# Performance work log

Hardware: AMD Instinct MI355X
Metric: run time of the kernel (lower is better)

## Reference

```python
import jax, jax.numpy as jnp
import numpy as np

EMB = 1024
HEADS = 16
HEAD_SIZE = EMB // HEADS  # 64
B, T = 2, 2048


def setup_inputs() -> dict:
    key = jax.random.key(0)
    k1, k2, k3 = jax.random.split(key, 3)
    x = jax.random.normal(k1, (B, T, EMB), dtype=jnp.float32)
    # scale weights like typical init to keep logits sane
    w_qkv = jax.random.normal(k2, (EMB, 3 * EMB), dtype=jnp.float32) * (EMB ** -0.5)
    w_proj = jax.random.normal(k3, (EMB, EMB), dtype=jnp.float32) * (EMB ** -0.5)
    b_proj = jnp.zeros((EMB,), dtype=jnp.float32)
    return {"x": x, "w_qkv": w_qkv, "w_proj": w_proj, "b_proj": b_proj}


def reference(x, w_qkv, w_proj, b_proj):
    Bb, Tt, C = x.shape
    qkv = x @ w_qkv  # [B,T,3C]
    q, k, v = jnp.split(qkv, 3, axis=-1)
    # [B,H,T,hs]
    q = q.reshape(Bb, Tt, HEADS, HEAD_SIZE).transpose(0, 2, 1, 3)
    k = k.reshape(Bb, Tt, HEADS, HEAD_SIZE).transpose(0, 2, 1, 3)
    v = v.reshape(Bb, Tt, HEADS, HEAD_SIZE).transpose(0, 2, 1, 3)
    scale = HEAD_SIZE ** -0.5
    wei = jnp.einsum('bhqd,bhkd->bhqk', q, k) * scale  # [B,H,T,T]
    causal = jnp.tril(jnp.ones((Tt, Tt), dtype=bool))
    wei = jnp.where(causal, wei, -jnp.inf)
    wei = jax.nn.softmax(wei, axis=-1)
    out = jnp.einsum('bhqk,bhkd->bhqd', wei, v)  # [B,H,T,hs]
    out = out.transpose(0, 2, 1, 3).reshape(Bb, Tt, C)
    out = out @ w_proj + b_proj
    return out
```

## Files before the change

### kernel.cpp

```cpp
#include <hip/hip_runtime.h>
#include <hip/hip_bf16.h>

typedef __attribute__((ext_vector_type(8))) short short8;
typedef __attribute__((ext_vector_type(4))) float floatx4;

#define MFMA16(a, b, c) __builtin_amdgcn_mfma_f32_16x16x32_bf16((a), (b), (c), 0, 0, 0)
#define GLOBAL_AS __attribute__((address_space(1)))
#define LDS_AS __attribute__((address_space(3)))

__device__ __forceinline__ unsigned short f2bf(float x) {
  union { float f; unsigned u; } v; v.f = x;
  unsigned r = v.u + 0x7FFFu + ((v.u >> 16) & 1u);
  return (unsigned short)(r >> 16);
}

__device__ __forceinline__ short8 ld8(const unsigned short* p) {
  return *reinterpret_cast<const short8*>(p);
}

__device__ __forceinline__ void async_cp16(const unsigned short* g, unsigned short* l) {
  __builtin_amdgcn_global_load_lds((const GLOBAL_AS void*)g, (LDS_AS void*)l, 16, 0, 0);
}

__global__ __launch_bounds__(256) void k_prep(
    const float* __restrict__ x, unsigned short* __restrict__ xb,
    const float* __restrict__ w_qkv, unsigned short* __restrict__ wqkvT,
    const float* __restrict__ w_proj, unsigned short* __restrict__ wprojT) {
  __shared__ float tile[64][65];
  int bid = blockIdx.x, tid = threadIdx.x;
  if (bid < 4096) {
    int i = bid * 256 + tid;
    float4 f = reinterpret_cast<const float4*>(x)[i];
    union { unsigned short u[4]; unsigned long long v; } o;
    o.u[0] = f2bf(f.x); o.u[1] = f2bf(f.y); o.u[2] = f2bf(f.z); o.u[3] = f2bf(f.w);
    reinterpret_cast<unsigned long long*>(xb)[i] = o.v;
    return;
  }
  const float* in; unsigned short* out; int R, C, bx, by;
  if (bid < 4864) {
    int rel = bid - 4096;
    in = w_qkv; out = wqkvT; R = 1024; C = 3072; bx = rel % 48; by = rel / 48;
  } else {
    int rel = bid - 4864;
    in = w_proj; out = wprojT; R = 1024; C = 1024; bx = rel % 16; by = rel / 16;
  }
  int tx = tid & 63, ty = tid >> 6;
  int c0 = bx * 64, r0 = by * 64;
  for (int i = ty; i < 64; i += 4)
    tile[i][tx] = in[(size_t)(r0 + i) * C + c0 + tx];
  __syncthreads();
  for (int i = ty; i < 64; i += 4)
    out[(size_t)(c0 + i) * R + r0 + tx] = f2bf(tile[tx][i]);
}

__global__ __launch_bounds__(256) void k_gemm_qkv(
    const unsigned short* __restrict__ A, const unsigned short* __restrict__ Bt,
    unsigned short* __restrict__ qk, unsigned short* __restrict__ vT, int K) {
  __shared__ unsigned short As[128][64];
  __shared__ unsigned short Bs[128][64];
  int tid = threadIdx.x;
  int w = tid >> 6, lane = tid & 63, quad = lane >> 4, l16 = lane & 15;
  int wy = w >> 1, wx = w & 1;
  int rowB = blockIdx.y * 128, colB = blockIdx.x * 128;
  int srcRow = lane >> 3;
  int srcCol = (((lane & 7) ^ (srcRow & 7)) << 3);

  floatx4 acc[4][4];
  floatx4 zero4 = {0.f, 0.f, 0.f, 0.f};
#pragma unroll
  for (int mi = 0; mi < 4; ++mi)
#pragma unroll
    for (int ni = 0; ni < 4; ++ni) acc[mi][ni] = zero4;

  for (int kt = 0; kt < K; kt += 64) {
    __syncthreads();
#pragma unroll
    for (int i = 0; i < 4; ++i) {
      int r0 = w * 32 + i * 8;
      async_cp16(&A[(size_t)(rowB + r0 + srcRow) * K + kt + srcCol], &As[r0][0]);
      async_cp16(&Bt[(size_t)(colB + r0 + srcRow) * K + kt + srcCol], &Bs[r0][0]);
    }
    __syncthreads();
#pragma unroll
    for (int kh = 0; kh < 2; ++kh) {
      short8 af[4], bf_[4];
#pragma unroll
      for (int mi = 0; mi < 4; ++mi)
        af[mi] = ld8(&As[wy * 64 + mi * 16 + l16][((kh * 4 + quad) ^ (l16 & 7)) << 3]);
#pragma unroll
      for (int ni = 0; ni < 4; ++ni)
        bf_[ni] = ld8(&Bs[wx * 64 + ni * 16 + l16][((kh * 4 + quad) ^ (l16 & 7)) << 3]);
#pragma unroll
      for (int mi = 0; mi < 4; ++mi)
#pragma unroll
        for (int ni = 0; ni < 4; ++ni)
          acc[mi][ni] = MFMA16(af[mi], bf_[ni], acc[mi][ni]);
    }
  }

  if (colB < 2048) {
#pragma unroll
    for (int mi = 0; mi < 4; ++mi) {
      int row = rowB + wy * 64 + mi * 16 + quad * 4;
#pragma unroll
      for (int ni = 0; ni < 4; ++ni) {
        int col = colB + wx * 64 + ni * 16 + l16;
#pragma unroll
        for (int r = 0; r < 4; ++r)
          qk[(size_t)(row + r) * 2048 + col] = f2bf(acc[mi][ni][r]);
      }
    }
  } else {
#pragma unroll
    for (int mi = 0; mi < 4; ++mi) {
      int row = rowB + wy * 64 + mi * 16 + quad * 4;
      int b = row >> 11, t = row & 2047;
#pragma unroll
      for (int ni = 0; ni < 4; ++ni) {
        int hd = colB - 2048 + wx * 64 + ni * 16 + l16;
        union { unsigned short u[4]; unsigned long long v; } o;
#pragma unroll
        for (int r = 0; r < 4; ++r) o.u[r] = f2bf(acc[mi][ni][r]);
        *reinterpret_cast<unsigned long long*>(
            &vT[((size_t)(b * 16) * 64 + hd) * 2048 + t]) = o.v;
      }
    }
  }
}

__global__ __launch_bounds__(256) void k_gemm_proj(
    const unsigned short* __restrict__ A, const unsigned short* __restrict__ Bt,
    float* __restrict__ Cout, const float* __restrict__ bias, int M, int N, int K) {
  __shared__ unsigned short As[128][64];
  __shared__ unsigned short Bs[64][64];
  int tid = threadIdx.x;
  int w = tid >> 6, lane = tid & 63, quad = lane >> 4, l16 = lane & 15;
  int rowB = blockIdx.y * 128, colB = blockIdx.x * 64;
  int srcRow = lane >> 3;
  int srcCol = (((lane & 7) ^ (srcRow & 7)) << 3);

  floatx4 acc[2][4];
  floatx4 zero4 = {0.f, 0.f, 0.f, 0.f};
#pragma unroll
  for (int mi = 0; mi < 2; ++mi)
#pragma unroll
    for (int ni = 0; ni < 4; ++ni) acc[mi][ni] = zero4;

  for (int kt = 0; kt < K; kt += 64) {
    __syncthreads();
#pragma unroll
    for (int i = 0; i < 4; ++i) {
      int r0 = w * 32 + i * 8;
      async_cp16(&A[(size_t)(rowB + r0 + srcRow) * K + kt + srcCol], &As[r0][0]);
    }
#pragma unroll
    for (int i = 0; i < 2; ++i) {
      int r0 = w * 16 + i * 8;
      async_cp16(&Bt[(size_t)(colB + r0 + srcRow) * K + kt + srcCol], &Bs[r0][0]);
    }
    __syncthreads();
#pragma unroll
    for (int kh = 0; kh < 2; ++kh) {
      short8 af[2], bf_[4];
#pragma unroll
      for (int mi = 0; mi < 2; ++mi)
        af[mi] = ld8(&As[w * 32 + mi * 16 + l16][((kh * 4 + quad) ^ (l16 & 7)) << 3]);
#pragma unroll
      for (int ni = 0; ni < 4; ++ni)
        bf_[ni] = ld8(&Bs[ni * 16 + l16][((kh * 4 + quad) ^ (l16 & 7)) << 3]);
#pragma unroll
      for (int mi = 0; mi < 2; ++mi)
#pragma unroll
        for (int ni = 0; ni < 4; ++ni)
          acc[mi][ni] = MFMA16(af[mi], bf_[ni], acc[mi][ni]);
    }
  }

#pragma unroll
  for (int mi = 0; mi < 2; ++mi) {
    int row = rowB + w * 32 + mi * 16 + quad * 4;
#pragma unroll
    for (int ni = 0; ni < 4; ++ni) {
      int col = colB + ni * 16 + l16;
      float bv = bias[col];
#pragma unroll
      for (int r = 0; r < 4; ++r)
        Cout[(size_t)(row + r) * N + col] = acc[mi][ni][r] + bv;
    }
  }
}

__global__ __launch_bounds__(256) void k_attn(
    const unsigned short* __restrict__ qk, const unsigned short* __restrict__ vT,
    unsigned short* __restrict__ attn_out) {
  const int T = 2048, LD = 2048;
  __shared__ unsigned short Kt[128][72];
  __shared__ unsigned short Vt[64][136];
  __shared__ unsigned short Pt[4][2][16][76];

  int idx = blockIdx.x;
  int ip = (idx >> 3) & 15;
  int bh = (idx & 7) | ((idx >> 7) << 3);
  int b = bh >> 4, h = bh & 15;
  int tid = threadIdx.x, w = tid >> 6, lane = tid & 63;
  int quad = lane >> 4, l16 = lane & 15;

  const unsigned short* Qp = qk + (size_t)b * T * LD + h * 64;
  const unsigned short* Kp = Qp + 1024;
  const unsigned short* Vp = vT + (size_t)bh * 64 * T;

  const int q0s[2] = {ip * 64, (31 - ip) * 64};
  const int last64[2] = {ip, 31 - ip};
  int nt = (33 - ip) >> 1;

  short8 aq[2][2];
#pragma unroll
  for (int m = 0; m < 2; ++m) {
    const unsigned short* qrow = Qp + (size_t)(q0s[m] + w * 16 + l16) * LD + quad * 8;
    aq[m][0] = ld8(qrow);
    aq[m][1] = ld8(qrow + 32);
  }

  short8 ones8;
  {
    unsigned short o = 0x3F80;
#pragma unroll
    for (int j = 0; j < 8; ++j) ones8[j] = (short)o;
  }

  const float cscale = 0.125f * 1.44269504f;
  floatx4 o_acc[2][4], l_acc[2];
  floatx4 zero4 = {0.f, 0.f, 0.f, 0.f};
#pragma unroll
  for (int m = 0; m < 2; ++m) {
    l_acc[m] = zero4;
#pragma unroll
    for (int nd = 0; nd < 4; ++nd) o_acc[m][nd] = zero4;
  }

  int skR = tid >> 3, skC = (tid & 7) << 3;
  int svR = tid >> 4, svC = (tid & 15) << 3;

  short8 kreg[4], vreg[4];
#pragma unroll
  for (int j = 0; j < 4; ++j) {
    kreg[j] = ld8(&Kp[(size_t)(skR + j * 32) * LD + skC]);
    vreg[j] = ld8(&Vp[(size_t)(svR + j * 16) * T + svC]);
  }

  for (int kt = 0; kt < nt; ++kt) {
    __syncthreads();
#pragma unroll
    for (int j = 0; j < 4; ++j) {
      *reinterpret_cast<short8*>(&Kt[skR + j * 32][skC]) = kreg[j];
      *reinterpret_cast<short8*>(&Vt[svR + j * 16][svC]) = vreg[j];
    }
    __syncthreads();

    if (kt + 1 < nt) {
      int key0n = (kt + 1) * 128;
#pragma unroll
      for (int j = 0; j < 4; ++j) {
        kreg[j] = ld8(&Kp[(size_t)(key0n + skR + j * 32) * LD + skC]);
        vreg[j] = ld8(&Vp[(size_t)(svR + j * 16) * T + key0n + svC]);
      }
    }

#pragma unroll
    for (int hh = 0; hh < 2; ++hh) {
      int half = kt * 2 + hh;
      if (half > last64[1]) continue;
      bool act0 = (half <= last64[0]);
      int key0 = half * 64;
      int ko = hh * 64;

      floatx4 st[2][4];
#pragma unroll
      for (int kt4 = 0; kt4 < 4; ++kt4) {
        short8 ak0 = ld8(&Kt[ko + kt4 * 16 + l16][quad * 8]);
        short8 ak1 = ld8(&Kt[ko + kt4 * 16 + l16][32 + quad * 8]);
        st[1][kt4] = MFMA16(ak0, aq[1][0], zero4);
        st[1][kt4] = MFMA16(ak1, aq[1][1], st[1][kt4]);
        if (act0) {
          st[0][kt4] = MFMA16(ak0, aq[0][0], zero4);
          st[0][kt4] = MFMA16(ak1, aq[0][1], st[0][kt4]);
        }
      }

#pragma unroll
      for (int m = 0; m < 2; ++m) {
        if (m == 0 && !act0) continue;
        if (half == last64[m]) {
          int qlane = q0s[m] + w * 16 + l16;
#pragma unroll
          for (int kt4 = 0; kt4 < 4; ++kt4)
#pragma unroll
            for (int r = 0; r < 4; ++r)
              if (key0 + kt4 * 16 + quad * 4 + r > qlane) st[m][kt4][r] = -1e30f;
        }
#pragma unroll
        for (int kt4 = 0; kt4 < 4; ++kt4) {
          unsigned u[4];
#pragma unroll
          for (int r = 0; r < 4; ++r) {
            float p = __builtin_amdgcn_exp2f(fmaf(st[m][kt4][r], cscale, -16.f));
            u[r] = __float_as_uint(p) + 0x8000u;
          }
          unsigned lo = __builtin_amdgcn_perm(u[1], u[0], 0x07060302u);
          unsigned hi = __builtin_amdgcn_perm(u[3], u[2], 0x07060302u);
          unsigned long long pv = ((unsigned long long)hi << 32) | lo;
          *reinterpret_cast<unsigned long long*>(
              &Pt[w][m][l16][kt4 * 16 + quad * 4]) = pv;
        }
      }

      short8 pa[2][2];
      pa[1][0] = ld8(&Pt[w][1][l16][quad * 8]);
      pa[1][1] = ld8(&Pt[w][1][l16][32 + quad * 8]);
      if (act0) {
        pa[0][0] = ld8(&Pt[w][0][l16][quad * 8]);
        pa[0][1] = ld8(&Pt[w][0][l16][32 + quad * 8]);
      }
#pragma unroll
      for (int nd = 0; nd < 4; ++nd) {
        short8 bv0 = ld8(&Vt[nd * 16 + l16][ko + quad * 8]);
        short8 bv1 = ld8(&Vt[nd * 16 + l16][ko + 32 + quad * 8]);
        o_acc[1][nd] = MFMA16(pa[1][0], bv0, o_acc[1][nd]);
        o_acc[1][nd] = MFMA16(pa[1][1], bv1, o_acc[1][nd]);
        if (act0) {
          o_acc[0][nd] = MFMA16(pa[0][0], bv0, o_acc[0][nd]);
          o_acc[0][nd] = MFMA16(pa[0][1], bv1, o_acc[0][nd]);
        }
      }
      l_acc[1] = MFMA16(pa[1][0], ones8, l_acc[1]);
      l_acc[1] = MFMA16(pa[1][1], ones8, l_acc[1]);
      if (act0) {
        l_acc[0] = MFMA16(pa[0][0], ones8, l_acc[0]);
        l_acc[0] = MFMA16(pa[0][1], ones8, l_acc[0]);
      }
    }
  }

#pragma unroll
  for (int m = 0; m < 2; ++m)
#pragma unroll
    for (int nd = 0; nd < 4; ++nd)
#pragma unroll
      for (int r = 0; r < 4; ++r) {
        int q = q0s[m] + w * 16 + quad * 4 + r;
        int d = nd * 16 + l16;
        attn_out[(size_t)(b * T + q) * 1024 + h * 64 + d] =
            f2bf(o_acc[m][nd][r] / l_acc[m][r]);
      }
}

extern "C" void kernel_launch(void* const* d_in, const int* in_sizes, int n_in,
                              void* d_out, int out_size, void* d_ws, size_t ws_size,
                              hipStream_t stream) {
  const float* x = (const float*)d_in[0];
  const float* w_qkv = (const float*)d_in[1];
  const float* w_proj = (const float*)d_in[2];
  const float* b_proj = (const float*)d_in[3];
  float* out = (float*)d_out;

  char* ws = (char*)d_ws;
  unsigned short* xb     = (unsigned short*)(ws);
  unsigned short* wqkvT  = (unsigned short*)(ws + (size_t)(8  << 20));
  unsigned short* wprojT = (unsigned short*)(ws + (size_t)(14 << 20));
  unsigned short* qkb    = (unsigned short*)(ws + (size_t)(16 << 20));
  unsigned short* attnb  = (unsigned short*)(ws + (size_t)(32 << 20));
  unsigned short* vTb    = (unsigned short*)(ws + (size_t)(40 << 20));

  k_prep<<<5120, 256, 0, stream>>>(x, xb, w_qkv, wqkvT, w_proj, wprojT);
  k_gemm_qkv<<<dim3(3072 / 128, 4096 / 128), 256, 0, stream>>>(
      xb, wqkvT, qkb, vTb, 1024);
  k_attn<<<512, 256, 0, stream>>>(qkb, vTb, attnb);
  k_gemm_proj<<<dim3(1024 / 64, 4096 / 128), 256, 0, stream>>>(
      attnb, wprojT, out, b_proj, 4096, 1024, 1024);
}
```

Before: 184.9 us.

## Split attention KV range across two blocks with split-K reduction via atomic counter

Each paired query tile's key range is split into two halves handled by separate blocks, doubling the grid to 1024 blocks. Each block writes unnormalized fp32 partial O and row sums to workspace. The second block to finish, detected by an atomic counter reset in the prep kernel, merges both partials and writes bf16 output. The KV tile shrinks to 64 keys to cut LDS use, and launch bounds request 4 blocks per SM. This aims at better occupancy and load balance at the cost of extra global traffic for the partials and a fence-plus-atomic reduction.

```diff
diff --git a/kernel.cpp b/kernel.cpp
--- a/kernel.cpp
+++ b/kernel.cpp
@@ -25,9 +25,14 @@
 __global__ __launch_bounds__(256) void k_prep(
     const float* __restrict__ x, unsigned short* __restrict__ xb,
     const float* __restrict__ w_qkv, unsigned short* __restrict__ wqkvT,
-    const float* __restrict__ w_proj, unsigned short* __restrict__ wprojT) {
+    const float* __restrict__ w_proj, unsigned short* __restrict__ wprojT,
+    int* __restrict__ counters) {
   __shared__ float tile[64][65];
   int bid = blockIdx.x, tid = threadIdx.x;
+  if (bid == 0) {
+    counters[tid] = 0;
+    counters[tid + 256] = 0;
+  }
   if (bid < 4096) {
     int i = bid * 256 + tid;
     float4 f = reinterpret_cast<const float4*>(x)[i];
@@ -190,18 +195,24 @@
   }
 }
 
-__global__ __launch_bounds__(256) void k_attn(
+__global__ __launch_bounds__(256, 4) void k_attn(
     const unsigned short* __restrict__ qk, const unsigned short* __restrict__ vT,
-    unsigned short* __restrict__ attn_out) {
+    unsigned short* __restrict__ attn_out,
+    float* __restrict__ o_part, float* __restrict__ l_part,
+    int* __restrict__ counters) {
   const int T = 2048, LD = 2048;
-  __shared__ unsigned short Kt[128][72];
-  __shared__ unsigned short Vt[64][136];
+  __shared__ unsigned short Kt[64][72];
+  __shared__ unsigned short Vt[64][72];
   __shared__ unsigned short Pt[4][2][16][76];
+  __shared__ int done;
 
   int idx = blockIdx.x;
-  int ip = (idx >> 3) & 15;
-  int bh = (idx & 7) | ((idx >> 7) << 3);
+  int hf = (idx >> 3) & 1;
+  int ip = (idx >> 4) & 15;
+  int bh = (idx & 7) | ((idx >> 8) << 3);
   int b = bh >> 4, h = bh & 15;
+  int pid = bh * 16 + ip;
+  int slot = pid * 2 + hf;
   int tid = threadIdx.x, w = tid >> 6, lane = tid & 63;
   int quad = lane >> 4, l16 = lane & 15;
 
@@ -211,7 +222,10 @@
 
   const int q0s[2] = {ip * 64, (31 - ip) * 64};
   const int last64[2] = {ip, 31 - ip};
-  int nt = (33 - ip) >> 1;
+  int NH = 32 - ip;
+  int hsplit = (ip >= 8) ? 9 : 16 - ip;
+  int h0 = hf ? hsplit : 0;
+  int h1 = hf ? NH : hsplit;
 
   short8 aq[2][2];
 #pragma unroll
@@ -239,119 +253,148 @@
   }
 
   int skR = tid >> 3, skC = (tid & 7) << 3;
-  int svR = tid >> 4, svC = (tid & 15) << 3;
-
-  short8 kreg[4], vreg[4];
-#pragma unroll
-  for (int j = 0; j < 4; ++j) {
-    kreg[j] = ld8(&Kp[(size_t)(skR + j * 32) * LD + skC]);
-    vreg[j] = ld8(&Vp[(size_t)(svR + j * 16) * T + svC]);
-  }
-
-  for (int kt = 0; kt < nt; ++kt) {
-    __syncthreads();
-#pragma unroll
-    for (int j = 0; j < 4; ++j) {
+
+  short8 kreg[2], vreg[2];
+#pragma unroll
+  for (int j = 0; j < 2; ++j) {
+    kreg[j] = ld8(&Kp[(size_t)(h0 * 64 + skR + j * 32) * LD + skC]);
+    vreg[j] = ld8(&Vp[(size_t)(skR + j * 32) * T + h0 * 64 + skC]);
+  }
+
+  for (int half = h0; half < h1; ++half) {
+    __syncthreads();
+#pragma unroll
+    for (int j = 0; j < 2; ++j) {
       *reinterpret_cast<short8*>(&Kt[skR + j * 32][skC]) = kreg[j];
-      *reinterpret_cast<short8*>(&Vt[svR + j * 16][svC]) = vreg[j];
-    }
-    __syncthreads();
-
-    if (kt + 1 < nt) {
-      int key0n = (kt + 1) * 128;
-#pragma unroll
-      for (int j = 0; j < 4; ++j) {
+      *reinterpret_cast<short8*>(&Vt[skR + j * 32][skC]) = vreg[j];
+    }
+    __syncthreads();
+
+    if (half + 1 < h1) {
+      int key0n = (half + 1) * 64;
+#pragma unroll
+      for (int j = 0; j < 2; ++j) {
         kreg[j] = ld8(&Kp[(size_t)(key0n + skR + j * 32) * LD + skC]);
-        vreg[j] = ld8(&Vp[(size_t)(svR + j * 16) * T + key0n + svC]);
-      }
-    }
-
-#pragma unroll
-    for (int hh = 0; hh < 2; ++hh) {
-      int half = kt * 2 + hh;
-      if (half > last64[1]) continue;
-      bool act0 = (half <= last64[0]);
-      int key0 = half * 64;
-      int ko = hh * 64;
-
-      floatx4 st[2][4];
+        vreg[j] = ld8(&Vp[(size_t)(skR + j * 32) * T + key0n + skC]);
+      }
+    }
+
+    bool act0 = (half <= last64[0]);
+    int key0 = half * 64;
+
+    floatx4 st[2][4];
+#pragma unroll
+    for (int kt4 = 0; kt4 < 4; ++kt4) {
+      short8 ak0 = ld8(&Kt[kt4 * 16 + l16][quad * 8]);
+      short8 ak1 = ld8(&Kt[kt4 * 16 + l16][32 + quad * 8]);
+      st[1][kt4] = MFMA16(ak0, aq[1][0], zero4);
+      st[1][kt4] = MFMA16(ak1, aq[1][1], st[1][kt4]);
+      if (act0) {
+        st[0][kt4] = MFMA16(ak0, aq[0][0], zero4);
+        st[0][kt4] = MFMA16(ak1, aq[0][1], st[0][kt4]);
+      }
+    }
+
+#pragma unroll
+    for (int m = 0; m < 2; ++m) {
+      if (m == 0 && !act0) continue;
+      if (half == last64[m]) {
+        int qlane = q0s[m] + w * 16 + l16;
+#pragma unroll
+        for (int kt4 = 0; kt4 < 4; ++kt4)
+#pragma unroll
+          for (int r = 0; r < 4; ++r)
+            if (key0 + kt4 * 16 + quad * 4 + r > qlane) st[m][kt4][r] = -1e30f;
+      }
 #pragma unroll
       for (int kt4 = 0; kt4 < 4; ++kt4) {
-        short8 ak0 = ld8(&Kt[ko + kt4 * 16 + l16][quad * 8]);
-        short8 ak1 = ld8(&Kt[ko + kt4 * 16 + l16][32 + quad * 8]);
-        st[1][kt4] = MFMA16(ak0, aq[1][0], zero4);
-        st[1][kt4] = MFMA16(ak1, aq[1][1], st[1][kt4]);
-        if (act0) {
-          st[0][kt4] = MFMA16(ak0, aq[0][0], zero4);
-          st[0][kt4] = MFMA16(ak1, aq[0][1], st[0][kt4]);
+        unsigned u[4];
+#pragma unroll
+        for (int r = 0; r < 4; ++r) {
+          float p = __builtin_amdgcn_exp2f(fmaf(st[m][kt4][r], cscale, -16.f));
+          u[r] = __float_as_uint(p) + 0x8000u;
         }
-      }
-
-#pragma unroll
-      for (int m = 0; m < 2; ++m) {
-        if (m == 0 && !act0) continue;
-        if (half == last64[m]) {
-          int qlane = q0s[m] + w * 16 + l16;
-#pragma unroll
-          for (int kt4 = 0; kt4 < 4; ++kt4)
-#pragma unroll
-            for (int r = 0; r < 4; ++r)
-              if (key0 + kt4 * 16 + quad * 4 + r > qlane) st[m][kt4][r] = -1e30f;
-        }
-#pragma unroll
-        for (int kt4 = 0; kt4 < 4; ++kt4) {
-          unsigned u[4];
-#pragma unroll
-          for (int r = 0; r < 4; ++r) {
-            float p = __builtin_amdgcn_exp2f(fmaf(st[m][kt4][r], cscale, -16.f));
-            u[r] = __float_as_uint(p) + 0x8000u;
-          }
-          unsigned lo = __builtin_amdgcn_perm(u[1], u[0], 0x07060302u);
-          unsigned hi = __builtin_amdgcn_perm(u[3], u[2], 0x07060302u);
-          unsigned long long pv = ((unsigned long long)hi << 32) | lo;
-          *reinterpret_cast<unsigned long long*>(
-              &Pt[w][m][l16][kt4 * 16 + quad * 4]) = pv;
-        }
-      }
-
-      short8 pa[2][2];
-      pa[1][0] = ld8(&Pt[w][1][l16][quad * 8]);
-      pa[1][1] = ld8(&Pt[w][1][l16][32 + quad * 8]);
+        unsigned lo = __builtin_amdgcn_perm(u[1], u[0], 0x07060302u);
+        unsigned hi = __builtin_amdgcn_perm(u[3], u[2], 0x07060302u);
+        unsigned long long pv = ((unsigned long long)hi << 32) | lo;
+        *reinterpret_cast<unsigned long long*>(
+            &Pt[w][m][l16][kt4 * 16 + quad * 4]) = pv;
+      }
+    }
+
+    short8 pa[2][2];
+    pa[1][0] = ld8(&Pt[w][1][l16][quad * 8]);
+    pa[1][1] = ld8(&Pt[w][1][l16][32 + quad * 8]);
+    if (act0) {
+      pa[0][0] = ld8(&Pt[w][0][l16][quad * 8]);
+      pa[0][1] = ld8(&Pt[w][0][l16][32 + quad * 8]);
+    }
+#pragma unroll
+    for (int nd = 0; nd < 4; ++nd) {
+      short8 bv0 = ld8(&Vt[nd * 16 + l16][quad * 8]);
+      short8 bv1 = ld8(&Vt[nd * 16 + l16][32 + quad * 8]);
+      o_acc[1][nd] = MFMA16(pa[1][0], bv0, o_acc[1][nd]);
+      o_acc[1][nd] = MFMA16(pa[1][1], bv1, o_acc[1][nd]);
       if (act0) {
-        pa[0][0] = ld8(&Pt[w][0][l16][quad * 8]);
-        pa[0][1] = ld8(&Pt[w][0][l16][32 + quad * 8]);
-      }
-#pragma unroll
-      for (int nd = 0; nd < 4; ++nd) {
-        short8 bv0 = ld8(&Vt[nd * 16 + l16][ko + quad * 8]);
-        short8 bv1 = ld8(&Vt[nd * 16 + l16][ko + 32 + quad * 8]);
-        o_acc[1][nd] = MFMA16(pa[1][0], bv0, o_acc[1][nd]);
-        o_acc[1][nd] = MFMA16(pa[1][1], bv1, o_acc[1][nd]);
-        if (act0) {
-          o_acc[0][nd] = MFMA16(pa[0][0], bv0, o_acc[0][nd]);
-          o_acc[0][nd] = MFMA16(pa[0][1], bv1, o_acc[0][nd]);
-        }
-      }
-      l_acc[1] = MFMA16(pa[1][0], ones8, l_acc[1]);
-      l_acc[1] = MFMA16(pa[1][1], ones8, l_acc[1]);
-      if (act0) {
-        l_acc[0] = MFMA16(pa[0][0], ones8, l_acc[0]);
-        l_acc[0] = MFMA16(pa[0][1], ones8, l_acc[0]);
-      }
-    }
-  }
-
+        o_acc[0][nd] = MFMA16(pa[0][0], bv0, o_acc[0][nd]);
+        o_acc[0][nd] = MFMA16(pa[0][1], bv1, o_acc[0][nd]);
+      }
+    }
+    l_acc[1] = MFMA16(pa[1][0], ones8, l_acc[1]);
+    l_acc[1] = MFMA16(pa[1][1], ones8, l_acc[1]);
+    if (act0) {
+      l_acc[0] = MFMA16(pa[0][0], ones8, l_acc[0]);
+      l_acc[0] = MFMA16(pa[0][1], ones8, l_acc[0]);
+    }
+  }
+
+  float* OP = o_part + (size_t)slot * (2 * 64 * 64);
+  float* LP = l_part + (size_t)slot * (2 * 64);
 #pragma unroll
   for (int m = 0; m < 2; ++m)
 #pragma unroll
     for (int nd = 0; nd < 4; ++nd)
 #pragma unroll
-      for (int r = 0; r < 4; ++r) {
-        int q = q0s[m] + w * 16 + quad * 4 + r;
-        int d = nd * 16 + l16;
-        attn_out[(size_t)(b * T + q) * 1024 + h * 64 + d] =
-            f2bf(o_acc[m][nd][r] / l_acc[m][r]);
-      }
+      for (int r = 0; r < 4; ++r)
+        OP[(m * 64 + w * 16 + quad * 4 + r) * 64 + nd * 16 + l16] = o_acc[m][nd][r];
+  if (l16 == 0)
+#pragma unroll
+    for (int m = 0; m < 2; ++m)
+#pragma unroll
+      for (int r = 0; r < 4; ++r)
+        LP[m * 64 + w * 16 + quad * 4 + r] = l_acc[m][r];
+
+  __threadfence();
+  __syncthreads();
+  if (tid == 0) done = atomicAdd(&counters[pid], 1);
+  __syncthreads();
+  if (done != 1) return;
+
+  __threadfence();
+  const float* PA = o_part + (size_t)(pid * 2) * (2 * 64 * 64);
+  const float* PB = PA + 2 * 64 * 64;
+  const float* LA = l_part + (size_t)(pid * 2) * (2 * 64);
+  const float* LB = LA + 2 * 64;
+#pragma unroll
+  for (int m = 0; m < 2; ++m) {
+    int qg0 = q0s[m];
+#pragma unroll
+    for (int pass = 0; pass < 4; ++pass) {
+      int q = pass * 16 + (tid >> 4);
+      int d0 = (tid & 15) * 4;
+      int off = (m * 64 + q) * 64 + d0;
+      float4 a = *reinterpret_cast<const float4*>(&PA[off]);
+      float4 c = *reinterpret_cast<const float4*>(&PB[off]);
+      float rl = 1.0f / (LA[m * 64 + q] + LB[m * 64 + q]);
+      union { unsigned short u[4]; unsigned long long v; } ob;
+      ob.u[0] = f2bf((a.x + c.x) * rl);
+      ob.u[1] = f2bf((a.y + c.y) * rl);
+      ob.u[2] = f2bf((a.z + c.z) * rl);
+      ob.u[3] = f2bf((a.w + c.w) * rl);
+      *reinterpret_cast<unsigned long long*>(
+          &attn_out[(size_t)(b * T + qg0 + q) * 1024 + h * 64 + d0]) = ob.v;
+    }
+  }
 }
 
 extern "C" void kernel_launch(void* const* d_in, const int* in_sizes, int n_in,
@@ -370,11 +413,14 @@
   unsigned short* qkb    = (unsigned short*)(ws + (size_t)(16 << 20));
   unsigned short* attnb  = (unsigned short*)(ws + (size_t)(32 << 20));
   unsigned short* vTb    = (unsigned short*)(ws + (size_t)(40 << 20));
-
-  k_prep<<<5120, 256, 0, stream>>>(x, xb, w_qkv, wqkvT, w_proj, wprojT);
+  float*          o_part = (float*)(ws + (size_t)(48 << 20));
+  float*          l_part = (float*)(ws + (size_t)(80 << 20));
+  int*            counters = (int*)(ws + (size_t)(80 << 20) + (512 << 10));
+
+  k_prep<<<5120, 256, 0, stream>>>(x, xb, w_qkv, wqkvT, w_proj, wprojT, counters);
   k_gemm_qkv<<<dim3(3072 / 128, 4096 / 128), 256, 0, stream>>>(
       xb, wqkvT, qkb, vTb, 1024);
-  k_attn<<<512, 256, 0, stream>>>(qkb, vTb, attnb);
+  k_attn<<<1024, 256, 0, stream>>>(qkb, vTb, attnb, o_part, l_part, counters);
   k_gemm_proj<<<dim3(1024 / 64, 4096 / 128), 256, 0, stream>>>(
       attnb, wprojT, out, b_proj, 4096, 1024, 1024);
 }
```

Result: slower. 414.1 us (+124.0%).

## Split paired causal attention blocks into one 64-row query tile per block

Applied to the files above, without the earlier changes.

Each attention block previously handled two paired query tiles (ip and 31-ip) to balance causal work, streaming 128-key tiles. Now each block handles a single 64-row query tile with 64-key tiles, and the grid doubles to 1024 blocks. A new block-index mapping interleaves short and long tiles and rotates their order to keep load balanced across CUs. This lowers per-block LDS and register use and gives more blocks to schedule, at the cost of per-block work that varies with position, reloading K/V once per query tile instead of once per pair, and more barriers per unit of work.

```diff
diff --git a/kernel.cpp b/kernel.cpp
--- a/kernel.cpp
+++ b/kernel.cpp
@@ -194,13 +194,16 @@
     const unsigned short* __restrict__ qk, const unsigned short* __restrict__ vT,
     unsigned short* __restrict__ attn_out) {
   const int T = 2048, LD = 2048;
-  __shared__ unsigned short Kt[128][72];
-  __shared__ unsigned short Vt[64][136];
-  __shared__ unsigned short Pt[4][2][16][76];
+  __shared__ unsigned short Kt[64][72];
+  __shared__ unsigned short Vt[64][72];
+  __shared__ unsigned short Pt[4][16][76];
 
   int idx = blockIdx.x;
-  int ip = (idx >> 3) & 15;
-  int bh = (idx & 7) | ((idx >> 7) << 3);
+  int s = idx >> 3;
+  int r = s >> 5, p = s & 31;
+  int pp = (r & 2) ? ((p + 16) & 31) : p;
+  int j = (r & 1) ? (31 - pp) : pp;
+  int bh = (idx & 7) * 4 + r;
   int b = bh >> 4, h = bh & 15;
   int tid = threadIdx.x, w = tid >> 6, lane = tid & 63;
   int quad = lane >> 4, l16 = lane & 15;
@@ -209,149 +212,114 @@
   const unsigned short* Kp = Qp + 1024;
   const unsigned short* Vp = vT + (size_t)bh * 64 * T;
 
-  const int q0s[2] = {ip * 64, (31 - ip) * 64};
-  const int last64[2] = {ip, 31 - ip};
-  int nt = (33 - ip) >> 1;
-
-  short8 aq[2][2];
-#pragma unroll
-  for (int m = 0; m < 2; ++m) {
-    const unsigned short* qrow = Qp + (size_t)(q0s[m] + w * 16 + l16) * LD + quad * 8;
-    aq[m][0] = ld8(qrow);
-    aq[m][1] = ld8(qrow + 32);
+  int q0 = j * 64;
+  int nt = j + 1;
+
+  short8 aq[2];
+  {
+    const unsigned short* qrow = Qp + (size_t)(q0 + w * 16 + l16) * LD + quad * 8;
+    aq[0] = ld8(qrow);
+    aq[1] = ld8(qrow + 32);
   }
 
   short8 ones8;
   {
     unsigned short o = 0x3F80;
 #pragma unroll
-    for (int j = 0; j < 8; ++j) ones8[j] = (short)o;
+    for (int i = 0; i < 8; ++i) ones8[i] = (short)o;
   }
 
   const float cscale = 0.125f * 1.44269504f;
-  floatx4 o_acc[2][4], l_acc[2];
+  floatx4 o_acc[4], l_acc;
   floatx4 zero4 = {0.f, 0.f, 0.f, 0.f};
-#pragma unroll
-  for (int m = 0; m < 2; ++m) {
-    l_acc[m] = zero4;
-#pragma unroll
-    for (int nd = 0; nd < 4; ++nd) o_acc[m][nd] = zero4;
-  }
+  l_acc = zero4;
+#pragma unroll
+  for (int nd = 0; nd < 4; ++nd) o_acc[nd] = zero4;
 
   int skR = tid >> 3, skC = (tid & 7) << 3;
-  int svR = tid >> 4, svC = (tid & 15) << 3;
-
-  short8 kreg[4], vreg[4];
-#pragma unroll
-  for (int j = 0; j < 4; ++j) {
-    kreg[j] = ld8(&Kp[(size_t)(skR + j * 32) * LD + skC]);
-    vreg[j] = ld8(&Vp[(size_t)(svR + j * 16) * T + svC]);
-  }
-
-  for (int kt = 0; kt < nt; ++kt) {
-    __syncthreads();
-#pragma unroll
-    for (int j = 0; j < 4; ++j) {
-      *reinterpret_cast<short8*>(&Kt[skR + j * 32][skC]) = kreg[j];
-      *reinterpret_cast<short8*>(&Vt[svR + j * 16][svC]) = vreg[j];
-    }
-    __syncthreads();
-
-    if (kt + 1 < nt) {
-      int key0n = (kt + 1) * 128;
-#pragma unroll
-      for (int j = 0; j < 4; ++j) {
-        kreg[j] = ld8(&Kp[(size_t)(key0n + skR + j * 32) * LD + skC]);
-        vreg[j] = ld8(&Vp[(size_t)(svR + j * 16) * T + key0n + svC]);
+
+  short8 kreg[2], vreg[2];
+#pragma unroll
+  for (int i = 0; i < 2; ++i) {
+    kreg[i] = ld8(&Kp[(size_t)(skR + i * 32) * LD + skC]);
+    vreg[i] = ld8(&Vp[(size_t)(skR + i * 32) * T + skC]);
+  }
+
+  for (int half = 0; half < nt; ++half) {
+    __syncthreads();
+#pragma unroll
+    for (int i = 0; i < 2; ++i) {
+      *reinterpret_cast<short8*>(&Kt[skR + i * 32][skC]) = kreg[i];
+      *reinterpret_cast<short8*>(&Vt[skR + i * 32][skC]) = vreg[i];
+    }
+    __syncthreads();
+
+    if (half + 1 < nt) {
+      int key0n = (half + 1) * 64;
+#pragma unroll
+      for (int i = 0; i < 2; ++i) {
+        kreg[i] = ld8(&Kp[(size_t)(key0n + skR + i * 32) * LD + skC]);
+        vreg[i] = ld8(&Vp[(size_t)(skR + i * 32) * T + key0n + skC]);
       }
     }
 
-#pragma unroll
-    for (int hh = 0; hh < 2; ++hh) {
-      int half = kt * 2 + hh;
-      if (half > last64[1]) continue;
-      bool act0 = (half <= last64[0]);
-      int key0 = half * 64;
-      int ko = hh * 64;
-
-      floatx4 st[2][4];
-#pragma unroll
-      for (int kt4 = 0; kt4 < 4; ++kt4) {
-        short8 ak0 = ld8(&Kt[ko + kt4 * 16 + l16][quad * 8]);
-        short8 ak1 = ld8(&Kt[ko + kt4 * 16 + l16][32 + quad * 8]);
-        st[1][kt4] = MFMA16(ak0, aq[1][0], zero4);
-        st[1][kt4] = MFMA16(ak1, aq[1][1], st[1][kt4]);
-        if (act0) {
-          st[0][kt4] = MFMA16(ak0, aq[0][0], zero4);
-          st[0][kt4] = MFMA16(ak1, aq[0][1], st[0][kt4]);
-        }
+    int key0 = half * 64;
+
+    floatx4 st[4];
+#pragma unroll
+    for (int kt4 = 0; kt4 < 4; ++kt4) {
+      short8 ak0 = ld8(&Kt[kt4 * 16 + l16][quad * 8]);
+      short8 ak1 = ld8(&Kt[kt4 * 16 + l16][32 + quad * 8]);
+      st[kt4] = MFMA16(ak0, aq[0], zero4);
+      st[kt4] = MFMA16(ak1, aq[1], st[kt4]);
+    }
+
+    if (half == j) {
+      int qlane = q0 + w * 16 + l16;
+#pragma unroll
+      for (int kt4 = 0; kt4 < 4; ++kt4)
+#pragma unroll
+        for (int rr = 0; rr < 4; ++rr)
+          if (key0 + kt4 * 16 + quad * 4 + rr > qlane) st[kt4][rr] = -1e30f;
+    }
+
+#pragma unroll
+    for (int kt4 = 0; kt4 < 4; ++kt4) {
+      unsigned u[4];
+#pragma unroll
+      for (int rr = 0; rr < 4; ++rr) {
+        float pe = __builtin_amdgcn_exp2f(fmaf(st[kt4][rr], cscale, -16.f));
+        u[rr] = __float_as_uint(pe) + 0x8000u;
       }
-
-#pragma unroll
-      for (int m = 0; m < 2; ++m) {
-        if (m == 0 && !act0) continue;
-        if (half == last64[m]) {
-          int qlane = q0s[m] + w * 16 + l16;
-#pragma unroll
-          for (int kt4 = 0; kt4 < 4; ++kt4)
-#pragma unroll
-            for (int r = 0; r < 4; ++r)
-              if (key0 + kt4 * 16 + quad * 4 + r > qlane) st[m][kt4][r] = -1e30f;
-        }
-#pragma unroll
-        for (int kt4 = 0; kt4 < 4; ++kt4) {
-          unsigned u[4];
-#pragma unroll
-          for (int r = 0; r < 4; ++r) {
-            float p = __builtin_amdgcn_exp2f(fmaf(st[m][kt4][r], cscale, -16.f));
-            u[r] = __float_as_uint(p) + 0x8000u;
-          }
-          unsigned lo = __builtin_amdgcn_perm(u[1], u[0], 0x07060302u);
-          unsigned hi = __builtin_amdgcn_perm(u[3], u[2], 0x07060302u);
-          unsigned long long pv = ((unsigned long long)hi << 32) | lo;
-          *reinterpret_cast<unsigned long long*>(
-              &Pt[w][m][l16][kt4 * 16 + quad * 4]) = pv;
-        }
-      }
-
-      short8 pa[2][2];
-      pa[1][0] = ld8(&Pt[w][1][l16][quad * 8]);
-      pa[1][1] = ld8(&Pt[w][1][l16][32 + quad * 8]);
-      if (act0) {
-        pa[0][0] = ld8(&Pt[w][0][l16][quad * 8]);
-        pa[0][1] = ld8(&Pt[w][0][l16][32 + quad * 8]);
-      }
-#pragma unroll
-      for (int nd = 0; nd < 4; ++nd) {
-        short8 bv0 = ld8(&Vt[nd * 16 + l16][ko + quad * 8]);
-        short8 bv1 = ld8(&Vt[nd * 16 + l16][ko + 32 + quad * 8]);
-        o_acc[1][nd] = MFMA16(pa[1][0], bv0, o_acc[1][nd]);
-        o_acc[1][nd] = MFMA16(pa[1][1], bv1, o_acc[1][nd]);
-        if (act0) {
-          o_acc[0][nd] = MFMA16(pa[0][0], bv0, o_acc[0][nd]);
-          o_acc[0][nd] = MFMA16(pa[0][1], bv1, o_acc[0][nd]);
-        }
-      }
-      l_acc[1] = MFMA16(pa[1][0], ones8, l_acc[1]);
-      l_acc[1] = MFMA16(pa[1][1], ones8, l_acc[1]);
-      if (act0) {
-        l_acc[0] = MFMA16(pa[0][0], ones8, l_acc[0]);
-        l_acc[0] = MFMA16(pa[0][1], ones8, l_acc[0]);
-      }
-    }
-  }
-
-#pragma unroll
-  for (int m = 0; m < 2; ++m)
-#pragma unroll
-    for (int nd = 0; nd < 4; ++nd)
-#pragma unroll
-      for (int r = 0; r < 4; ++r) {
-        int q = q0s[m] + w * 16 + quad * 4 + r;
-        int d = nd * 16 + l16;
-        attn_out[(size_t)(b * T + q) * 1024 + h * 64 + d] =
-            f2bf(o_acc[m][nd][r] / l_acc[m][r]);
-      }
+      unsigned lo = __builtin_amdgcn_perm(u[1], u[0], 0x07060302u);
+      unsigned hi = __builtin_amdgcn_perm(u[3], u[2], 0x07060302u);
+      unsigned long long pv = ((unsigned long long)hi << 32) | lo;
+      *reinterpret_cast<unsigned long long*>(
+          &Pt[w][l16][kt4 * 16 + quad * 4]) = pv;
+    }
+
+    short8 pa0 = ld8(&Pt[w][l16][quad * 8]);
+    short8 pa1 = ld8(&Pt[w][l16][32 + quad * 8]);
+#pragma unroll
+    for (int nd = 0; nd < 4; ++nd) {
+      short8 bv0 = ld8(&Vt[nd * 16 + l16][quad * 8]);
+      short8 bv1 = ld8(&Vt[nd * 16 + l16][32 + quad * 8]);
+      o_acc[nd] = MFMA16(pa0, bv0, o_acc[nd]);
+      o_acc[nd] = MFMA16(pa1, bv1, o_acc[nd]);
+    }
+    l_acc = MFMA16(pa0, ones8, l_acc);
+    l_acc = MFMA16(pa1, ones8, l_acc);
+  }
+
+#pragma unroll
+  for (int nd = 0; nd < 4; ++nd)
+#pragma unroll
+    for (int rr = 0; rr < 4; ++rr) {
+      int q = q0 + w * 16 + quad * 4 + rr;
+      int d = nd * 16 + l16;
+      attn_out[(size_t)(b * T + q) * 1024 + h * 64 + d] =
+          f2bf(o_acc[nd][rr] / l_acc[rr]);
+    }
 }
 
 extern "C" void kernel_launch(void* const* d_in, const int* in_sizes, int n_in,
@@ -374,7 +342,7 @@
   k_prep<<<5120, 256, 0, stream>>>(x, xb, w_qkv, wqkvT, w_proj, wprojT);
   k_gemm_qkv<<<dim3(3072 / 128, 4096 / 128), 256, 0, stream>>>(
       xb, wqkvT, qkb, vTb, 1024);
-  k_attn<<<512, 256, 0, stream>>>(qkb, vTb, attnb);
+  k_attn<<<1024, 256, 0, stream>>>(qkb, vTb, attnb);
   k_gemm_proj<<<dim3(1024 / 64, 4096 / 128), 256, 0, stream>>>(
       attnb, wprojT, out, b_proj, 4096, 1024, 1024);
 }
```

Measured after the change: 183.7 us. No clear change (-0.6%).
